# Kernel optimization log

Measured on AMD Instinct MI355X. Metric: run time of the kernel, lower is better.

## Reference

```python
import jax, jax.numpy as jnp
import numpy as np

N = 8192        # nodes
D_IN = 512      # input features
H = 256         # hidden (GAT out_features)
D_OUT = 16      # output classes
K = 16          # num clusters/classes
LRELU_SLOPE = 0.2
MASK_FILL = -9e15
EDGE_P = 0.002  # sparsity of random adjacency


def setup_inputs() -> dict:
    key = jax.random.key(0)
    k1, k2, k3, k4, k5, k6 = jax.random.split(key, 6)
    x = jax.random.normal(k1, (N, D_IN), dtype=jnp.float32)
    # binary adjacency with self loops (module only tests adj > 0; support reused as propagation matrix)
    adj = (jax.random.uniform(k2, (N, N)) < EDGE_P).astype(jnp.float32)
    adj = jnp.maximum(adj, jnp.eye(N, dtype=jnp.float32))
    C_a = jax.random.normal(k3, (K, H), dtype=jnp.float32)
    # learned parameters (xavier-ish scale)
    W = jax.random.normal(k4, (D_IN, H), dtype=jnp.float32) * (1.414 * (2.0 / (D_IN + H)) ** 0.5)
    a = jax.random.normal(k5, (2 * H, 1), dtype=jnp.float32) * (1.414 * (2.0 / (2 * H + 1)) ** 0.5)
    W_gcn = jax.random.normal(k6, (H, D_OUT), dtype=jnp.float32)
    return {"x": x, "adj": adj, "C_a": C_a, "W": W, "a": a, "W_gcn": W_gcn}


def _clust_score(Z, C):
    # score[n,k] = exp(-||Z_n - C_k||) normalized over k (beta = 1)
    d = jnp.sqrt(((Z[:, None, :] - C[None, :, :]) ** 2).sum(-1))  # [N,K]
    s = jnp.exp(-d) + 1e-10
    return s / s.sum(axis=1, keepdims=True)


def reference(x, adj, C_a, W, a, W_gcn):
    h = W.shape[1]
    # --- GAT layer ---
    Wh = x @ W                                   # [N,H]
    Wh1 = Wh @ a[:h, :]                          # [N,1]
    Wh2 = Wh @ a[h:, :]                          # [N,1]
    e = jax.nn.leaky_relu(Wh1 + Wh2.T, LRELU_SLOPE)   # [N,N]
    att = jax.nn.softmax(jnp.where(adj > 0, e, MASK_FILL), axis=1)
    Z_0 = att @ Wh                               # h_prime, [N,H]
    gatoutput = jax.nn.elu(Z_0)
    # --- cluster score on detached Z_0 (update=False path) ---
    score = _clust_score(jax.lax.stop_gradient(Z_0), C_a)
    # --- GCN layer (B_1 = I, so Z_1 = F_1) ---
    F_1 = jax.nn.relu(adj @ (gatoutput @ W_gcn))  # [N,D_OUT]
    output = F_1
    Z_1 = F_1
    return (output, Z_1, Z_0, score)
```

## Files before the change

### kernel.cpp

```cpp
#include <hip/hip_runtime.h>
#include <hip/hip_bf16.h>

#define N_NODES 8192
#define D_IN    512
#define H       256
#define D_OUT   16
#define K_CL    16
#define MAXN    96

#define OUT_OFF 0
#define Z1_OFF  131072
#define Z0_OFF  262144
#define SC_OFF  2359296

typedef unsigned int   u32;
typedef unsigned short u16;

__device__ __forceinline__ float load_in(const void* p, int bf, size_t idx) {
    if (bf) { u32 w = ((const u16*)p)[idx]; return __uint_as_float(w << 16); }
    return ((const float*)p)[idx];
}
__device__ __forceinline__ void store_out(void* p, int bf, size_t idx, float v) {
    if (bf) ((__hip_bfloat16*)p)[idx] = __float2bfloat16(v);
    else    ((float*)p)[idx] = v;
}

__global__ void k_detect(const u32* __restrict__ adjw, int* __restrict__ flag) {
    int t = blockIdx.x * 256 + threadIdx.x;
    int hit = 0;
    #pragma unroll 4
    for (int i = 0; i < 64; i++)
        if (adjw[(size_t)t + (size_t)i * 16384] == 0x00003F80u) hit = 1;
    if (hit) atomicOr(flag, 1);
}

__global__ void k_prep_small(const void* av, const void* C_a, const void* Wgcn,
                             const int* __restrict__ flag,
                             float* a_f, float* Ca_f, float* Wg_f) {
    int bf = *flag;
    int i = blockIdx.x * 256 + threadIdx.x;
    if (i < 512)        a_f[i]         = load_in(av,   bf, i);
    else if (i < 4608)  Ca_f[i - 512]  = load_in(C_a,  bf, i - 512);
    else if (i < 8704)  Wg_f[i - 4608] = load_in(Wgcn, bf, i - 4608);
}

__global__ __launch_bounds__(256) void k_gemm_wh(
    const void* __restrict__ xraw, const void* __restrict__ wraw,
    const int* __restrict__ flag, float* __restrict__ Wh)
{
    int bf = *flag;
    __shared__ float xs[32][68];
    __shared__ float ws_[32][68];
    int tid = threadIdx.x;
    int bm = blockIdx.x >> 2, bn = blockIdx.x & 3;
    int m0 = bm * 64, n0 = bn * 64;
    int tx = tid & 15, ty = tid >> 4;
    float acc[4][4] = {};

    for (int k0 = 0; k0 < D_IN; k0 += 32) {
        {
            int r = tid >> 2, kq = (tid & 3) * 8;
            size_t base = (size_t)(m0 + r) * D_IN + k0 + kq;
            float v[8];
            if (bf) {
                uint4 raw = *(const uint4*)((const u16*)xraw + base);
                u32 rr[4] = {raw.x, raw.y, raw.z, raw.w};
                #pragma unroll
                for (int q = 0; q < 4; q++) {
                    v[2*q]   = __uint_as_float(rr[q] << 16);
                    v[2*q+1] = __uint_as_float(rr[q] & 0xFFFF0000u);
                }
            } else {
                float4 f0 = *(const float4*)((const float*)xraw + base);
                float4 f1 = *(const float4*)((const float*)xraw + base + 4);
                v[0]=f0.x; v[1]=f0.y; v[2]=f0.z; v[3]=f0.w;
                v[4]=f1.x; v[5]=f1.y; v[6]=f1.z; v[7]=f1.w;
            }
            #pragma unroll
            for (int u = 0; u < 8; u++) xs[kq + u][r] = v[u];
        }
        {
            int kk = tid >> 3, n8 = (tid & 7) * 8;
            size_t base = (size_t)(k0 + kk) * H + n0 + n8;
            if (bf) {
                uint4 raw = *(const uint4*)((const u16*)wraw + base);
                u32 rr[4] = {raw.x, raw.y, raw.z, raw.w};
                #pragma unroll
                for (int q = 0; q < 4; q++) {
                    ws_[kk][n8 + 2*q]   = __uint_as_float(rr[q] << 16);
                    ws_[kk][n8 + 2*q+1] = __uint_as_float(rr[q] & 0xFFFF0000u);
                }
            } else {
                float4 f0 = *(const float4*)((const float*)wraw + base);
                float4 f1 = *(const float4*)((const float*)wraw + base + 4);
                ws_[kk][n8+0]=f0.x; ws_[kk][n8+1]=f0.y; ws_[kk][n8+2]=f0.z; ws_[kk][n8+3]=f0.w;
                ws_[kk][n8+4]=f1.x; ws_[kk][n8+5]=f1.y; ws_[kk][n8+6]=f1.z; ws_[kk][n8+7]=f1.w;
            }
        }
        __syncthreads();
        #pragma unroll
        for (int kk = 0; kk < 32; kk++) {
            float4 a4 = *(const float4*)&xs[kk][ty * 4];
            float4 b4 = *(const float4*)&ws_[kk][tx * 4];
            float a[4] = {a4.x, a4.y, a4.z, a4.w};
            float b[4] = {b4.x, b4.y, b4.z, b4.w};
            #pragma unroll
            for (int i = 0; i < 4; i++)
                #pragma unroll
                for (int j = 0; j < 4; j++)
                    acc[i][j] += a[i] * b[j];
        }
        __syncthreads();
    }
    #pragma unroll
    for (int i = 0; i < 4; i++) {
        float4 o = {acc[i][0], acc[i][1], acc[i][2], acc[i][3]};
        *(float4*)&Wh[(size_t)(m0 + ty*4 + i) * H + n0 + tx*4] = o;
    }
}

__global__ __launch_bounds__(256) void k_wh12(
    const float* __restrict__ Wh, const float* __restrict__ a_f,
    float* __restrict__ Wh1, float* __restrict__ Wh2)
{
    int tid = threadIdx.x;
    int wave = tid >> 6, lane = tid & 63;
    int n = blockIdx.x * 4 + wave;
    float4 v  = *(const float4*)(Wh + (size_t)n * H + lane * 4);
    float4 a1 = *(const float4*)(a_f + lane * 4);
    float4 a2 = *(const float4*)(a_f + H + lane * 4);
    float s1 = v.x*a1.x + v.y*a1.y + v.z*a1.z + v.w*a1.w;
    float s2 = v.x*a2.x + v.y*a2.y + v.z*a2.z + v.w*a2.w;
    #pragma unroll
    for (int off = 32; off; off >>= 1) {
        s1 += __shfl_xor(s1, off);
        s2 += __shfl_xor(s2, off);
    }
    if (lane == 0) { Wh1[n] = s1; Wh2[n] = s2; }
}

__global__ __launch_bounds__(256) void k_gat_row(
    const void* __restrict__ adjraw, const int* __restrict__ flag,
    const float* __restrict__ Wh,
    const float* __restrict__ Wh1, const float* __restrict__ Wh2,
    const float* __restrict__ Ca_f, const float* __restrict__ Wg_f,
    float* __restrict__ Gf,
    int* __restrict__ nbr_cnt, u16* __restrict__ nbr_idx,
    void* __restrict__ dout)
{
    const int n = blockIdx.x;
    const int tid = threadIdx.x;
    const int bf = *flag;
    __shared__ int   s_cnt;
    __shared__ int   s_idx[MAXN];
    __shared__ float s_att[MAXN];
    __shared__ float s_z[H];
    __shared__ float s_g[H];
    __shared__ float s_red[256];
    __shared__ float s_sc[16];

    if (tid == 0) s_cnt = 0;
    __syncthreads();

    if (bf) {
        const u16* arow = (const u16*)adjraw + (size_t)n * N_NODES;
        #pragma unroll
        for (int it = 0; it < 4; it++) {
            int base = it * 2048 + tid * 8;
            uint4 raw = *(const uint4*)(arow + base);
            u32 rw[4] = {raw.x, raw.y, raw.z, raw.w};
            #pragma unroll
            for (int q = 0; q < 4; q++) {
                #pragma unroll
                for (int hh = 0; hh < 2; hh++) {
                    u32 u = (rw[q] >> (16 * hh)) & 0xFFFFu;
                    if (__uint_as_float(u << 16) > 0.f) {
                        int p = atomicAdd(&s_cnt, 1);
                        if (p < MAXN) s_idx[p] = base + q * 2 + hh;
                    }
                }
            }
        }
    } else {
        const float* arow = (const float*)adjraw + (size_t)n * N_NODES;
        #pragma unroll
        for (int it = 0; it < 8; it++) {
            int base = it * 1024 + tid * 4;
            float4 v = *(const float4*)(arow + base);
            float vv[4] = {v.x, v.y, v.z, v.w};
            #pragma unroll
            for (int q = 0; q < 4; q++) {
                if (vv[q] > 0.f) {
                    int p = atomicAdd(&s_cnt, 1);
                    if (p < MAXN) s_idx[p] = base + q;
                }
            }
        }
    }
    __syncthreads();
    const int cnt = min(s_cnt, MAXN);
    if (tid == 0) nbr_cnt[n] = cnt;
    if (tid < cnt) nbr_idx[(size_t)n * MAXN + tid] = (u16)s_idx[tid];

    float e = 0.f;
    if (tid < cnt) {
        float v = Wh1[n] + Wh2[s_idx[tid]];
        e = v > 0.f ? v : 0.2f * v;
    }
    s_red[tid] = (tid < cnt) ? e : -3e38f;
    __syncthreads();
    #pragma unroll
    for (int s = 128; s > 0; s >>= 1) {
        if (tid < s) s_red[tid] = fmaxf(s_red[tid], s_red[tid + s]);
        __syncthreads();
    }
    float m = s_red[0];
    __syncthreads();
    float wexp = (tid < cnt) ? expf(e - m) : 0.f;
    s_red[tid] = wexp;
    __syncthreads();
    #pragma unroll
    for (int s = 128; s > 0; s >>= 1) {
        if (tid < s) s_red[tid] += s_red[tid + s];
        __syncthreads();
    }
    float denom = s_red[0];
    if (tid < cnt) s_att[tid] = wexp / denom;
    __syncthreads();

    float acc = 0.f;
    for (int t = 0; t < cnt; t++)
        acc += s_att[t] * Wh[(size_t)s_idx[t] * H + tid];
    s_z[tid] = acc;
    store_out(dout, bf, (size_t)Z0_OFF + (size_t)n * H + tid, acc);
    s_g[tid] = acc > 0.f ? acc : expf(acc) - 1.f;
    __syncthreads();

    {
        int k = tid & 15, hb = (tid >> 4) * 16;
        float p = 0.f;
        #pragma unroll
        for (int i = 0; i < 16; i++) {
            float d = s_z[hb + i] - Ca_f[(size_t)k * H + hb + i];
            p += d * d;
        }
        s_red[tid] = p;
    }
    __syncthreads();
    if (tid < 16) {
        float d2 = 0.f;
        #pragma unroll
        for (int q = 0; q < 16; q++) d2 += s_red[q * 16 + tid];
        s_sc[tid] = expf(-sqrtf(d2)) + 1e-10f;
    }
    __syncthreads();
    if (tid < 16) {
        float tot = 0.f;
        #pragma unroll
        for (int q = 0; q < 16; q++) tot += s_sc[q];
        store_out(dout, bf, (size_t)SC_OFF + (size_t)n * K_CL + tid, s_sc[tid] / tot);
    }
    __syncthreads();

    {
        int o = tid & 15, hb = (tid >> 4) * 16;
        float p = 0.f;
        #pragma unroll
        for (int i = 0; i < 16; i++)
            p += s_g[hb + i] * Wg_f[(size_t)(hb + i) * D_OUT + o];
        s_red[tid] = p;
    }
    __syncthreads();
    if (tid < 16) {
        float g2 = 0.f;
        #pragma unroll
        for (int q = 0; q < 16; q++) g2 += s_red[q * 16 + tid];
        Gf[(size_t)n * D_OUT + tid] = g2;
    }
}

__global__ __launch_bounds__(256) void k_f1(
    const int* __restrict__ nbr_cnt, const u16* __restrict__ nbr_idx,
    const float* __restrict__ Gf, const int* __restrict__ flag,
    void* __restrict__ dout)
{
    int tid = threadIdx.x;
    int bf = *flag;
    int r = tid >> 4, o = tid & 15;
    int n = blockIdx.x * 16 + r;
    int cnt = nbr_cnt[n];
    const u16* idx = nbr_idx + (size_t)n * MAXN;
    float acc = 0.f;
    for (int t = 0; t < cnt; t++)
        acc += Gf[(size_t)idx[t] * D_OUT + o];
    acc = fmaxf(acc, 0.f);
    store_out(dout, bf, (size_t)OUT_OFF + (size_t)n * D_OUT + o, acc);
    store_out(dout, bf, (size_t)Z1_OFF  + (size_t)n * D_OUT + o, acc);
}

extern "C" void kernel_launch(void* const* d_in, const int* in_sizes, int n_in,
                              void* d_out, int out_size, void* d_ws, size_t ws_size,
                              hipStream_t stream) {
    const void* x    = d_in[0];
    const void* adj  = d_in[1];
    const void* C_a  = d_in[2];
    const void* W    = d_in[3];
    const void* av   = d_in[4];
    const void* Wgcn = d_in[5];

    char* wsp = (char*)d_ws;
    int*   flag = (int*)wsp;                   wsp += 256;
    float* Wh   = (float*)wsp;                 wsp += (size_t)N_NODES * H * 4;
    float* Wh1  = (float*)wsp;                 wsp += (size_t)N_NODES * 4;
    float* Wh2  = (float*)wsp;                 wsp += (size_t)N_NODES * 4;
    float* Gf   = (float*)wsp;                 wsp += (size_t)N_NODES * D_OUT * 4;
    int*   ncnt = (int*)wsp;                   wsp += (size_t)N_NODES * 4;
    u16*   nidx = (u16*)wsp;                   wsp += (size_t)N_NODES * MAXN * 2;
    float* a_f  = (float*)wsp;                 wsp += 2 * H * 4;
    float* Ca_f = (float*)wsp;                 wsp += (size_t)K_CL * H * 4;
    float* Wg_f = (float*)wsp;                 wsp += (size_t)H * D_OUT * 4;

    hipMemsetAsync(flag, 0, sizeof(int), stream);
    k_detect    <<<64, 256, 0, stream>>>((const u32*)adj, flag);
    k_prep_small<<<34, 256, 0, stream>>>(av, C_a, Wgcn, flag, a_f, Ca_f, Wg_f);
    k_gemm_wh   <<<512, 256, 0, stream>>>(x, W, flag, Wh);
    k_wh12      <<<N_NODES / 4, 256, 0, stream>>>(Wh, a_f, Wh1, Wh2);
    k_gat_row   <<<N_NODES, 256, 0, stream>>>(adj, flag, Wh, Wh1, Wh2, Ca_f, Wg_f,
                                              Gf, ncnt, nidx, d_out);
    k_f1        <<<N_NODES / 16, 256, 0, stream>>>(ncnt, nidx, Gf, flag, d_out);
}
```

Measured before the change: 456.9 us.

## Use bf16 MFMA for Wh GEMM, shuffle-based softmax reductions, unrolled gathers

On bf16 inputs, the Wh projection now runs on MFMA 16x16x32 bf16 instructions, reading a pre-transposed bf16 copy of W built by a new prep kernel. The GAT row kernel replaces its shared-memory tree reductions for softmax max and sum with wave shuffles plus a 4-entry cross-wave combine. The neighbor gather loops in the GAT and F1 kernels are unrolled by four to keep more loads in flight. The dtype-detect kernel is launched over more blocks with fewer iterations per thread. The costs are an extra kernel launch and a W transpose on every call, and the fp32 path keeps the old scalar GEMM.

```diff
diff --git a/kernel.cpp b/kernel.cpp
--- a/kernel.cpp
+++ b/kernel.cpp
@@ -15,6 +15,8 @@
 
 typedef unsigned int   u32;
 typedef unsigned short u16;
+typedef __attribute__((ext_vector_type(8))) short bf16x8;
+typedef __attribute__((ext_vector_type(4))) float f32x4;
 
 __device__ __forceinline__ float load_in(const void* p, int bf, size_t idx) {
     if (bf) { u32 w = ((const u16*)p)[idx]; return __uint_as_float(w << 16); }
@@ -29,8 +31,8 @@
     int t = blockIdx.x * 256 + threadIdx.x;
     int hit = 0;
     #pragma unroll 4
-    for (int i = 0; i < 64; i++)
-        if (adjw[(size_t)t + (size_t)i * 16384] == 0x00003F80u) hit = 1;
+    for (int i = 0; i < 16; i++)
+        if (adjw[(size_t)t + (size_t)i * 65536] == 0x00003F80u) hit = 1;
     if (hit) atomicOr(flag, 1);
 }
 
@@ -44,8 +46,19 @@
     else if (i < 8704)  Wg_f[i - 4608] = load_in(Wgcn, bf, i - 4608);
 }
 
+__global__ void k_prep_wt(const void* __restrict__ wraw,
+                          const int* __restrict__ flag, u16* __restrict__ Wt) {
+    int bf = *flag;
+    int idx = blockIdx.x * 256 + threadIdx.x;
+    int h = idx >> 9, k = idx & 511;
+    float v = load_in(wraw, bf, (size_t)k * H + h);
+    __hip_bfloat16 b = __float2bfloat16(v);
+    Wt[(size_t)h * D_IN + k] = *(u16*)&b;
+}
+
 __global__ __launch_bounds__(256) void k_gemm_wh(
     const void* __restrict__ xraw, const void* __restrict__ wraw,
+    const u16* __restrict__ Wt,
     const int* __restrict__ flag, float* __restrict__ Wh)
 {
     int bf = *flag;
@@ -54,48 +67,61 @@
     int tid = threadIdx.x;
     int bm = blockIdx.x >> 2, bn = blockIdx.x & 3;
     int m0 = bm * 64, n0 = bn * 64;
+
+    if (bf) {
+        int wave = tid >> 6, lane = tid & 63;
+        int wr = wave >> 1, wc = wave & 1;
+        int r0 = m0 + wr * 32, c0 = n0 + wc * 32;
+        int lr = lane & 15, lk = lane >> 4;
+        const u16* xp = (const u16*)xraw;
+        const u16* a0p = xp + (size_t)(r0 + lr)      * D_IN + lk * 8;
+        const u16* a1p = xp + (size_t)(r0 + 16 + lr) * D_IN + lk * 8;
+        const u16* b0p = Wt + (size_t)(c0 + lr)      * D_IN + lk * 8;
+        const u16* b1p = Wt + (size_t)(c0 + 16 + lr) * D_IN + lk * 8;
+        f32x4 acc[2][2] = {};
+        #pragma unroll 4
+        for (int k0 = 0; k0 < D_IN; k0 += 32) {
+            bf16x8 a0 = *(const bf16x8*)(a0p + k0);
+            bf16x8 a1 = *(const bf16x8*)(a1p + k0);
+            bf16x8 b0 = *(const bf16x8*)(b0p + k0);
+            bf16x8 b1 = *(const bf16x8*)(b1p + k0);
+            acc[0][0] = __builtin_amdgcn_mfma_f32_16x16x32_bf16(a0, b0, acc[0][0], 0, 0, 0);
+            acc[0][1] = __builtin_amdgcn_mfma_f32_16x16x32_bf16(a0, b1, acc[0][1], 0, 0, 0);
+            acc[1][0] = __builtin_amdgcn_mfma_f32_16x16x32_bf16(a1, b0, acc[1][0], 0, 0, 0);
+            acc[1][1] = __builtin_amdgcn_mfma_f32_16x16x32_bf16(a1, b1, acc[1][1], 0, 0, 0);
+        }
+        #pragma unroll
+        for (int i = 0; i < 2; i++) {
+            #pragma unroll
+            for (int reg = 0; reg < 4; reg++) {
+                int r = r0 + 16 * i + 4 * lk + reg;
+                Wh[(size_t)r * H + c0 + lr]      = acc[i][0][reg];
+                Wh[(size_t)r * H + c0 + 16 + lr] = acc[i][1][reg];
+            }
+        }
+        return;
+    }
+
     int tx = tid & 15, ty = tid >> 4;
     float acc[4][4] = {};
-
     for (int k0 = 0; k0 < D_IN; k0 += 32) {
         {
             int r = tid >> 2, kq = (tid & 3) * 8;
             size_t base = (size_t)(m0 + r) * D_IN + k0 + kq;
-            float v[8];
-            if (bf) {
-                uint4 raw = *(const uint4*)((const u16*)xraw + base);
-                u32 rr[4] = {raw.x, raw.y, raw.z, raw.w};
-                #pragma unroll
-                for (int q = 0; q < 4; q++) {
-                    v[2*q]   = __uint_as_float(rr[q] << 16);
-                    v[2*q+1] = __uint_as_float(rr[q] & 0xFFFF0000u);
-                }
-            } else {
-                float4 f0 = *(const float4*)((const float*)xraw + base);
-                float4 f1 = *(const float4*)((const float*)xraw + base + 4);
-                v[0]=f0.x; v[1]=f0.y; v[2]=f0.z; v[3]=f0.w;
-                v[4]=f1.x; v[5]=f1.y; v[6]=f1.z; v[7]=f1.w;
-            }
-            #pragma unroll
-            for (int u = 0; u < 8; u++) xs[kq + u][r] = v[u];
+            float4 f0 = *(const float4*)((const float*)xraw + base);
+            float4 f1 = *(const float4*)((const float*)xraw + base + 4);
+            xs[kq + 0][r] = f0.x; xs[kq + 1][r] = f0.y;
+            xs[kq + 2][r] = f0.z; xs[kq + 3][r] = f0.w;
+            xs[kq + 4][r] = f1.x; xs[kq + 5][r] = f1.y;
+            xs[kq + 6][r] = f1.z; xs[kq + 7][r] = f1.w;
         }
         {
             int kk = tid >> 3, n8 = (tid & 7) * 8;
             size_t base = (size_t)(k0 + kk) * H + n0 + n8;
-            if (bf) {
-                uint4 raw = *(const uint4*)((const u16*)wraw + base);
-                u32 rr[4] = {raw.x, raw.y, raw.z, raw.w};
-                #pragma unroll
-                for (int q = 0; q < 4; q++) {
-                    ws_[kk][n8 + 2*q]   = __uint_as_float(rr[q] << 16);
-                    ws_[kk][n8 + 2*q+1] = __uint_as_float(rr[q] & 0xFFFF0000u);
-                }
-            } else {
-                float4 f0 = *(const float4*)((const float*)wraw + base);
-                float4 f1 = *(const float4*)((const float*)wraw + base + 4);
-                ws_[kk][n8+0]=f0.x; ws_[kk][n8+1]=f0.y; ws_[kk][n8+2]=f0.z; ws_[kk][n8+3]=f0.w;
-                ws_[kk][n8+4]=f1.x; ws_[kk][n8+5]=f1.y; ws_[kk][n8+6]=f1.z; ws_[kk][n8+7]=f1.w;
-            }
+            float4 f0 = *(const float4*)((const float*)wraw + base);
+            float4 f1 = *(const float4*)((const float*)wraw + base + 4);
+            ws_[kk][n8+0]=f0.x; ws_[kk][n8+1]=f0.y; ws_[kk][n8+2]=f0.z; ws_[kk][n8+3]=f0.w;
+            ws_[kk][n8+4]=f1.x; ws_[kk][n8+5]=f1.y; ws_[kk][n8+6]=f1.z; ws_[kk][n8+7]=f1.w;
         }
         __syncthreads();
         #pragma unroll
@@ -207,30 +233,38 @@
         float v = Wh1[n] + Wh2[s_idx[tid]];
         e = v > 0.f ? v : 0.2f * v;
     }
-    s_red[tid] = (tid < cnt) ? e : -3e38f;
-    __syncthreads();
+    int lane = tid & 63, wv = tid >> 6;
+    float vmax = (tid < cnt) ? e : -3e38f;
     #pragma unroll
-    for (int s = 128; s > 0; s >>= 1) {
-        if (tid < s) s_red[tid] = fmaxf(s_red[tid], s_red[tid + s]);
-        __syncthreads();
-    }
-    float m = s_red[0];
-    __syncthreads();
+    for (int off = 32; off; off >>= 1) vmax = fmaxf(vmax, __shfl_xor(vmax, off));
+    if (lane == 0) s_red[wv] = vmax;
+    __syncthreads();
+    float m = fmaxf(fmaxf(s_red[0], s_red[1]), fmaxf(s_red[2], s_red[3]));
     float wexp = (tid < cnt) ? expf(e - m) : 0.f;
-    s_red[tid] = wexp;
-    __syncthreads();
+    float ssum = wexp;
     #pragma unroll
-    for (int s = 128; s > 0; s >>= 1) {
-        if (tid < s) s_red[tid] += s_red[tid + s];
-        __syncthreads();
-    }
-    float denom = s_red[0];
+    for (int off = 32; off; off >>= 1) ssum += __shfl_xor(ssum, off);
+    if (lane == 0) s_red[8 + wv] = ssum;
+    __syncthreads();
+    float denom = s_red[8] + s_red[9] + s_red[10] + s_red[11];
     if (tid < cnt) s_att[tid] = wexp / denom;
     __syncthreads();
 
     float acc = 0.f;
-    for (int t = 0; t < cnt; t++)
-        acc += s_att[t] * Wh[(size_t)s_idx[t] * H + tid];
+    {
+        int t = 0;
+        for (; t + 4 <= cnt; t += 4) {
+            int i0 = s_idx[t], i1 = s_idx[t+1], i2 = s_idx[t+2], i3 = s_idx[t+3];
+            float w0 = s_att[t], w1 = s_att[t+1], w2 = s_att[t+2], w3 = s_att[t+3];
+            float x0 = Wh[(size_t)i0 * H + tid];
+            float x1 = Wh[(size_t)i1 * H + tid];
+            float x2 = Wh[(size_t)i2 * H + tid];
+            float x3 = Wh[(size_t)i3 * H + tid];
+            acc += w0 * x0; acc += w1 * x1; acc += w2 * x2; acc += w3 * x3;
+        }
+        for (; t < cnt; t++)
+            acc += s_att[t] * Wh[(size_t)s_idx[t] * H + tid];
+    }
     s_z[tid] = acc;
     store_out(dout, bf, (size_t)Z0_OFF + (size_t)n * H + tid, acc);
     s_g[tid] = acc > 0.f ? acc : expf(acc) - 1.f;
@@ -291,7 +325,16 @@
     int cnt = nbr_cnt[n];
     const u16* idx = nbr_idx + (size_t)n * MAXN;
     float acc = 0.f;
-    for (int t = 0; t < cnt; t++)
+    int t = 0;
+    for (; t + 4 <= cnt; t += 4) {
+        int i0 = idx[t], i1 = idx[t+1], i2 = idx[t+2], i3 = idx[t+3];
+        float g0 = Gf[(size_t)i0 * D_OUT + o];
+        float g1 = Gf[(size_t)i1 * D_OUT + o];
+        float g2 = Gf[(size_t)i2 * D_OUT + o];
+        float g3 = Gf[(size_t)i3 * D_OUT + o];
+        acc += g0; acc += g1; acc += g2; acc += g3;
+    }
+    for (; t < cnt; t++)
         acc += Gf[(size_t)idx[t] * D_OUT + o];
     acc = fmaxf(acc, 0.f);
     store_out(dout, bf, (size_t)OUT_OFF + (size_t)n * D_OUT + o, acc);
@@ -319,11 +362,13 @@
     float* a_f  = (float*)wsp;                 wsp += 2 * H * 4;
     float* Ca_f = (float*)wsp;                 wsp += (size_t)K_CL * H * 4;
     float* Wg_f = (float*)wsp;                 wsp += (size_t)H * D_OUT * 4;
+    u16*   Wt   = (u16*)wsp;                   wsp += (size_t)H * D_IN * 2;
 
     hipMemsetAsync(flag, 0, sizeof(int), stream);
-    k_detect    <<<64, 256, 0, stream>>>((const u32*)adj, flag);
+    k_detect    <<<256, 256, 0, stream>>>((const u32*)adj, flag);
     k_prep_small<<<34, 256, 0, stream>>>(av, C_a, Wgcn, flag, a_f, Ca_f, Wg_f);
-    k_gemm_wh   <<<512, 256, 0, stream>>>(x, W, flag, Wh);
+    k_prep_wt   <<<512, 256, 0, stream>>>(W, flag, Wt);
+    k_gemm_wh   <<<512, 256, 0, stream>>>(x, W, Wt, flag, Wh);
     k_wh12      <<<N_NODES / 4, 256, 0, stream>>>(Wh, a_f, Wh1, Wh2);
     k_gat_row   <<<N_NODES, 256, 0, stream>>>(adj, flag, Wh, Wh1, Wh2, Ca_f, Wg_f,
                                               Gf, ncnt, nidx, d_out);
```

Result: faster. 443.9 us (-2.9%).
